# Performance work log

Measured on AMD Instinct MI355X. Metric: run time of the kernel, lower is better.

The kernel has to match this reference:

```python
import jax, jax.numpy as jnp
import numpy as np

N, E, G = 50000, 600000, 512   # nodes, edges, graphs
F, D, L = 128, 128, 3          # in_features, hidden dim, num_gc_layers
ED = D * L                      # embedding_dim (readout='concat')
C = 1.0                         # curvature
MIN_NORM = 1e-15
BALL_EPS = 4e-3                 # hgcn PoincareBall proj eps for float32


def _logmap0(p, c):
    sc = jnp.sqrt(c)
    n = jnp.clip(jnp.linalg.norm(p, axis=-1, keepdims=True), MIN_NORM, None)
    return p / (sc * n) * jnp.arctanh(jnp.clip(sc * n, -1 + 1e-15, 1 - 1e-15))


def _expmap0(u, c):
    sc = jnp.sqrt(c)
    n = jnp.clip(jnp.linalg.norm(u, axis=-1, keepdims=True), MIN_NORM, None)
    return jnp.tanh(sc * n) * u / (sc * n)


def _proj(x, c):
    n = jnp.clip(jnp.linalg.norm(x, axis=-1, keepdims=True), MIN_NORM, None)
    maxn = (1.0 - BALL_EPS) / jnp.sqrt(c)
    return jnp.where(n > maxn, x / n * maxn, x)


def _gcn(x, W, b, src, dst):
    h = x @ W
    deg = jax.ops.segment_sum(jnp.ones_like(dst, dtype=h.dtype), dst, num_segments=N) + 1.0
    dinv = deg ** -0.5
    msg = h[src] * (dinv[src] * dinv[dst])[:, None]           # [E, D]
    agg = jax.ops.segment_sum(msg, dst, num_segments=N) + h * (dinv * dinv)[:, None]
    return agg + b


def _encoder(x, Ws, bs, src, dst, batch):
    xs = []
    for W, b in zip(Ws, bs):
        x = jax.nn.relu(_gcn(x, W, b, src, dst))
        xs.append(x)
    # readout='concat' with global_add_pool
    g = jnp.concatenate([jax.ops.segment_sum(h, batch, num_segments=G) for h in xs], axis=1)
    return g, jnp.concatenate(xs, axis=1)


def _mlp(x, W1, W2):  # proj_head: Linear (no bias), ReLU, Linear (no bias)
    return jax.nn.relu(x @ W1) @ W2


def setup_inputs() -> dict:
    key = jax.random.key(0)
    ks = jax.random.split(key, 24)

    def xav(k, i, o):
        return jax.random.normal(k, (i, o), dtype=jnp.float32) * np.float32(np.sqrt(2.0 / (i + o)))

    inp = {
        'x':   jax.random.normal(ks[0], (N, F), dtype=jnp.float32) * 1e-3,  # points inside the ball
        'x_s': jax.random.normal(ks[1], (N, F), dtype=jnp.float32) * 1e-3,
        'src': jax.random.randint(ks[2], (E,), 0, N, dtype=jnp.int32),
        'dst': jax.random.randint(ks[3], (E,), 0, N, dtype=jnp.int32),
        'batch': jnp.sort(jax.random.randint(ks[4], (N,), 0, G, dtype=jnp.int32)),
        # feature-branch GCN encoder
        'Wf0': xav(ks[5], F, D), 'Wf1': xav(ks[6], D, D), 'Wf2': xav(ks[7], D, D),
        'bf0': jnp.zeros((D,), jnp.float32), 'bf1': jnp.zeros((D,), jnp.float32), 'bf2': jnp.zeros((D,), jnp.float32),
        # structure-branch GCN encoder
        'Ws0': xav(ks[8], F, D), 'Ws1': xav(ks[9], D, D), 'Ws2': xav(ks[10], D, D),
        'bs0': jnp.zeros((D,), jnp.float32), 'bs1': jnp.zeros((D,), jnp.float32), 'bs2': jnp.zeros((D,), jnp.float32),
        # proj heads (biases removed by init_emb)
        'P1': xav(ks[11], ED, ED), 'P2': xav(ks[12], ED, ED),
        'G1': xav(ks[13], 2 * ED, ED), 'G2': xav(ks[14], ED, ED),
    }
    return inp


def reference(x, x_s, Wf0, Wf1, Wf2, bf0, bf1, bf2, Ws0, Ws1, Ws2, bs0, bs1, bs2, P1, P2, G1, G2, src, dst, batch):
    xt_f = _logmap0(x, C)
    xt_s = _logmap0(x_s, C)
    g_f, n_f = _encoder(xt_f, (Wf0, Wf1, Wf2), (bf0, bf1, bf2), src, dst, batch)
    g_s, n_s = _encoder(xt_s, (Ws0, Ws1, Ws2), (bs0, bs1, bs2), src, dst, batch)
    g = _mlp(jnp.concatenate((g_f, g_s), axis=1), G1, G2)
    e = lambda t: _proj(_expmap0(t, C), C)
    return (e(g), e(_mlp(g_f, P1, P2)), e(_mlp(n_f, P1, P2)), e(_mlp(g_s, P1, P2)), e(_mlp(n_s, P1, P2)))
```

## Files before the change

### kernel.cpp

```cpp
#include <hip/hip_runtime.h>
#include <math.h>

#define N_NODES 50000
#define N_EDGES 600000
#define N_GRAPHS 512
#define F_IN 128
#define D_HID 128
#define EDIM 384
#define M_ALL (N_NODES + N_GRAPHS)

typedef __attribute__((ext_vector_type(8))) short bf16x8;
typedef __attribute__((ext_vector_type(4))) float f32x4;

static __device__ __forceinline__ float wave_reduce_sum(float s) {
#pragma unroll
  for (int off = 32; off > 0; off >>= 1) s += __shfl_xor(s, off, 64);
  return s;
}

static __device__ __forceinline__ short f2b(float f) {
  unsigned u = __float_as_uint(f);
  unsigned r = (u + 0x7FFFu + ((u >> 16) & 1u)) >> 16;
  return (short)r;
}

static __device__ __forceinline__ float b2f(short s) {
  return __uint_as_float(((unsigned)(unsigned short)s) << 16);
}


__global__ void hist_kernel(const int* __restrict__ dst, int* __restrict__ cnt) {
  int i = blockIdx.x * blockDim.x + threadIdx.x;
  if (i < N_EDGES) atomicAdd(&cnt[dst[i]], 1);
}

__global__ void gptr_kernel(const int* __restrict__ batch, int* __restrict__ gptr) {
  int g = blockIdx.x * blockDim.x + threadIdx.x;
  if (g > N_GRAPHS) return;
  int lo = 0, hi = N_NODES;
  while (lo < hi) { int mid = (lo + hi) >> 1; if (batch[mid] < g) lo = mid + 1; else hi = mid; }
  gptr[g] = lo;
}


#define SCAN_BS 256
#define SCAN_NB ((N_NODES + SCAN_BS - 1) / SCAN_BS)

__global__ __launch_bounds__(SCAN_BS) void scan1_kernel(const int* __restrict__ cnt,
                                                        int* __restrict__ row_ptr,
                                                        int* __restrict__ bsum) {
  __shared__ int wsum[4];
  int tid = threadIdx.x, lane = tid & 63, wid = tid >> 6;
  int idx = blockIdx.x * SCAN_BS + tid;
  int v = (idx < N_NODES) ? cnt[idx] : 0;
  int x = v;
#pragma unroll
  for (int off = 1; off < 64; off <<= 1) {
    int t = __shfl_up(x, off, 64);
    if (lane >= off) x += t;
  }
  if (lane == 63) wsum[wid] = x;
  __syncthreads();
  int pre = 0, tot = 0;
#pragma unroll
  for (int w = 0; w < 4; ++w) { int s = wsum[w]; tot += s; if (w < wid) pre += s; }
  if (idx < N_NODES) row_ptr[idx + 1] = x + pre;
  if (tid == 0) bsum[blockIdx.x] = tot;
}

__global__ __launch_bounds__(SCAN_BS) void scan2_kernel(const int* __restrict__ bsum,
                                                        int* __restrict__ boffs) {
  __shared__ int wsum[4];
  int tid = threadIdx.x, lane = tid & 63, wid = tid >> 6;
  int v = (tid < SCAN_NB) ? bsum[tid] : 0;
  int x = v;
#pragma unroll
  for (int off = 1; off < 64; off <<= 1) {
    int t = __shfl_up(x, off, 64);
    if (lane >= off) x += t;
  }
  if (lane == 63) wsum[wid] = x;
  __syncthreads();
  int pre = 0;
#pragma unroll
  for (int w = 0; w < 4; ++w) { int s = wsum[w]; if (w < wid) pre += s; }
  if (tid < SCAN_NB) boffs[tid] = x + pre - v;
}

__global__ __launch_bounds__(SCAN_BS) void scan3_kernel(const int* __restrict__ cnt,
                                                        const int* __restrict__ boffs,
                                                        int* __restrict__ row_ptr,
                                                        int* __restrict__ cursor) {
  int idx = blockIdx.x * SCAN_BS + threadIdx.x;
  if (idx >= N_NODES) return;
  int val = row_ptr[idx + 1] + boffs[blockIdx.x];
  row_ptr[idx + 1] = val;
  cursor[idx] = val - cnt[idx];
  if (idx == 0) row_ptr[0] = 0;
}

__global__ void dinv_kernel(const int* __restrict__ cnt, float* __restrict__ dinv) {
  int i = blockIdx.x * blockDim.x + threadIdx.x;
  if (i < N_NODES) dinv[i] = 1.0f / sqrtf((float)(cnt[i] + 1));
}

__global__ void scatter_kernel(const int* __restrict__ src, const int* __restrict__ dst,
                               const float* __restrict__ dinv, int* __restrict__ cursor,
                               int* __restrict__ col, float* __restrict__ ew) {
  int e = blockIdx.x * blockDim.x + threadIdx.x;
  if (e >= N_EDGES) return;
  int s = src[e], d = dst[e];
  int pos = atomicAdd(&cursor[d], 1);
  col[pos] = s;
  ew[pos] = dinv[s] * dinv[d];
}


struct WcSeg { const float* W; short* Wt; int K; int Nc; };
struct WcArgs { WcSeg seg[10]; };

__global__ void wconv_all_kernel(WcArgs a) {
  int sidx = blockIdx.y;
  WcSeg s = a.seg[sidx];
  int i = blockIdx.x * blockDim.x + threadIdx.x;
  if (i >= s.K * s.Nc) return;
  int k = i / s.Nc, n = i - k * s.Nc;
  s.Wt[(size_t)n * s.K + k] = f2b(s.W[i]);
}


__global__ __launch_bounds__(256) void logmap2_kernel(const float* __restrict__ x,
                                                      const float* __restrict__ x_s,
                                                      short* __restrict__ Ab) {
  int w = blockIdx.x * 4 + (threadIdx.x >> 6);
  int lane = threadIdx.x & 63;
  if (w >= 2 * N_NODES) return;
  int br = (w >= N_NODES) ? 1 : 0;
  int row = br ? (w - N_NODES) : w;
  const float* xr = (br ? x_s : x) + (size_t)row * F_IN;
  float2 v = *(const float2*)(xr + lane * 2);
  float s = wave_reduce_sum(v.x * v.x + v.y * v.y);
  float n = sqrtf(s);
  float nc = fmaxf(n, 1e-15f);
  float f = atanhf(fminf(nc, 0.9999999f)) / nc;
  short2 o; o.x = f2b(v.x * f); o.y = f2b(v.y * f);
  *(short2*)(Ab + (size_t)row * 256 + br * 128 + lane * 2) = o;
}


__global__ __launch_bounds__(256) void agg2_kernel(const short* __restrict__ Xin, int lda,
                                                   const float* __restrict__ dinv,
                                                   const int* __restrict__ row_ptr,
                                                   const int* __restrict__ col,
                                                   const float* __restrict__ ew,
                                                   short* __restrict__ Xa) {
  int node = blockIdx.x * 4 + (threadIdx.x >> 6);
  int lane = threadIdx.x & 63;
  if (node >= N_NODES) return;
  float di = dinv[node];
  float wsf = di * di;
  short4 sv = *(const short4*)(Xin + (size_t)node * lda + lane * 4);
  float a0 = b2f(sv.x) * wsf, a1 = b2f(sv.y) * wsf, a2 = b2f(sv.z) * wsf, a3 = b2f(sv.w) * wsf;
  int s = row_ptr[node], e = row_ptr[node + 1];
  int j = s;
  for (; j + 4 <= e; j += 4) {
    int c0 = col[j], c1 = col[j + 1], c2 = col[j + 2], c3 = col[j + 3];
    float w0 = ew[j], w1 = ew[j + 1], w2 = ew[j + 2], w3 = ew[j + 3];
    short4 v0 = *(const short4*)(Xin + (size_t)c0 * lda + lane * 4);
    short4 v1 = *(const short4*)(Xin + (size_t)c1 * lda + lane * 4);
    short4 v2 = *(const short4*)(Xin + (size_t)c2 * lda + lane * 4);
    short4 v3 = *(const short4*)(Xin + (size_t)c3 * lda + lane * 4);
    a0 += b2f(v0.x) * w0; a1 += b2f(v0.y) * w0; a2 += b2f(v0.z) * w0; a3 += b2f(v0.w) * w0;
    a0 += b2f(v1.x) * w1; a1 += b2f(v1.y) * w1; a2 += b2f(v1.z) * w1; a3 += b2f(v1.w) * w1;
    a0 += b2f(v2.x) * w2; a1 += b2f(v2.y) * w2; a2 += b2f(v2.z) * w2; a3 += b2f(v2.w) * w2;
    a0 += b2f(v3.x) * w3; a1 += b2f(v3.y) * w3; a2 += b2f(v3.z) * w3; a3 += b2f(v3.w) * w3;
  }
  for (; j < e; ++j) {
    float w0 = ew[j];
    short4 v0 = *(const short4*)(Xin + (size_t)col[j] * lda + lane * 4);
    a0 += b2f(v0.x) * w0; a1 += b2f(v0.y) * w0; a2 += b2f(v0.z) * w0; a3 += b2f(v0.w) * w0;
  }
  short4 o; o.x = f2b(a0); o.y = f2b(a1); o.z = f2b(a2); o.w = f2b(a3);
  *(short4*)(Xa + (size_t)node * 256 + lane * 4) = o;
}


#define LDK 40

struct GemmZArgs {
  const short* A[2];
  const short* Bt[2];
  const float* bias[2];
  short* Cb[2];
  float* Cf[2];
  float* Cf2[2];
  int lda, ldc, M, Nc, K, kexp, do_relu, split;
};

__global__ __launch_bounds__(256) void mfma_gemmz_kernel(GemmZArgs g) {
  __shared__ __align__(16) short As[128 * LDK];
  __shared__ __align__(16) short Bs[128 * LDK];
  int z = blockIdx.z;
  const short* __restrict__ A = g.A[z];
  const short* __restrict__ Bt = g.Bt[z];
  int tid = threadIdx.x;
  int wave = tid >> 6, lane = tid & 63;
  int wr = (wave >> 1) * 64, wc = (wave & 1) * 64;
  int q = lane >> 4, m = lane & 15;
  int row0 = blockIdx.x * 128, col0 = blockIdx.y * 128;
  f32x4 acc[4][4] = {};
  for (int k0 = 0; k0 < g.K; k0 += 32) {
#pragma unroll
    for (int p = 0; p < 2; ++p) {
      int idx = p * 256 + tid;
      int r = idx >> 2, kc = (idx & 3) * 8;
      int gr = row0 + r;
      int kk = k0 + kc;
      int acol = g.kexp ? (kk + ((kk >> 7) << 7)) : kk;
      float4 v = make_float4(0.f, 0.f, 0.f, 0.f);
      if (gr < g.M) v = *(const float4*)(A + (size_t)gr * g.lda + acol);
      *(float4*)(As + r * LDK + kc) = v;
      float4 w = *(const float4*)(Bt + (size_t)(col0 + r) * g.K + kk);
      *(float4*)(Bs + r * LDK + kc) = w;
    }
    __syncthreads();
    bf16x8 af[4], bfr[4];
#pragma unroll
    for (int i = 0; i < 4; ++i) {
      af[i]  = *(const bf16x8*)(As + (wr + i * 16 + m) * LDK + q * 8);
      bfr[i] = *(const bf16x8*)(Bs + (wc + i * 16 + m) * LDK + q * 8);
    }
#pragma unroll
    for (int i = 0; i < 4; ++i)
#pragma unroll
      for (int j = 0; j < 4; ++j)
        acc[i][j] = __builtin_amdgcn_mfma_f32_16x16x32_bf16(af[i], bfr[j], acc[i][j], 0, 0, 0);
    __syncthreads();
  }
  const float* __restrict__ bias = g.bias[z];
  short* __restrict__ Cb = g.Cb[z];
  float* __restrict__ Cf = g.Cf[z];
  float* __restrict__ Cf2 = g.Cf2[z];
#pragma unroll
  for (int i = 0; i < 4; ++i) {
#pragma unroll
    for (int r = 0; r < 4; ++r) {
      int rr = row0 + wr + i * 16 + q * 4 + r;
      if (rr >= g.M) continue;
#pragma unroll
      for (int j = 0; j < 4; ++j) {
        int cc = col0 + wc + j * 16 + m;
        float v = acc[i][j][r];
        if (bias) v += bias[cc];
        if (g.do_relu) v = fmaxf(v, 0.0f);
        if (Cb) Cb[(size_t)rr * g.ldc + cc] = f2b(v);
        else if (rr < g.split) Cf[(size_t)rr * g.Nc + cc] = v;
        else Cf2[(size_t)(rr - g.split) * g.Nc + cc] = v;
      }
    }
  }
}


__global__ __launch_bounds__(768) void pool2_kernel(const short* __restrict__ NB,
                                                    const int* __restrict__ gptr,
                                                    short* __restrict__ GCb,
                                                    short* __restrict__ nbappend) {
  int g = blockIdx.x, t = threadIdx.x;
  int s = gptr[g], e = gptr[g + 1];
  float acc = 0.0f;
  for (int i = s; i < e; ++i) acc += b2f(NB[(size_t)i * 768 + t]);
  short bv = f2b(acc);
  int l = t >> 8, rem = t & 255, b = rem >> 7, c = rem & 127;
  GCb[(size_t)g * 768 + b * 384 + l * 128 + c] = bv;
  nbappend[(size_t)g * 768 + t] = bv;
}


__global__ __launch_bounds__(256) void exp_proj_kernel(float* __restrict__ y, int nrows) {
  int row = blockIdx.x * 4 + (threadIdx.x >> 6);
  int lane = threadIdx.x & 63;
  if (row >= nrows) return;
  float* p = y + (size_t)row * EDIM;
  float v[6];
  float s = 0.0f;
#pragma unroll
  for (int j = 0; j < 6; ++j) { v[j] = p[lane + j * 64]; s += v[j] * v[j]; }
  s = wave_reduce_sum(s);
  float n = fmaxf(sqrtf(s), 1e-15f);
  float th = tanhf(n);
  float f = th / n;
  float n2 = fmaxf(th, 1e-15f);
  const float maxn = 1.0f - 4e-3f;
  if (n2 > maxn) f *= maxn / n2;
#pragma unroll
  for (int j = 0; j < 6; ++j) p[lane + j * 64] = v[j] * f;
}


extern "C" void kernel_launch(void* const* d_in, const int* in_sizes, int n_in,
                              void* d_out, int out_size, void* d_ws, size_t ws_size,
                              hipStream_t stream) {
  (void)in_sizes; (void)n_in; (void)out_size; (void)ws_size;
  const float* x   = (const float*)d_in[0];
  const float* x_s = (const float*)d_in[1];
  const int* src   = (const int*)d_in[2];
  const int* dst   = (const int*)d_in[3];
  const int* batch = (const int*)d_in[4];
  const float* Wf[3] = {(const float*)d_in[5], (const float*)d_in[6], (const float*)d_in[7]};
  const float* bf[3] = {(const float*)d_in[8], (const float*)d_in[9], (const float*)d_in[10]};
  const float* Wsb[3] = {(const float*)d_in[11], (const float*)d_in[12], (const float*)d_in[13]};
  const float* bs[3] = {(const float*)d_in[14], (const float*)d_in[15], (const float*)d_in[16]};
  const float* P1 = (const float*)d_in[17];
  const float* P2 = (const float*)d_in[18];
  const float* G1 = (const float*)d_in[19];
  const float* G2 = (const float*)d_in[20];
  float* out = (float*)d_out;

  char* w = (char*)d_ws;
  auto alloc = [&](size_t bytes) {
    char* p = w;
    w += (bytes + 255) & ~(size_t)255;
    return p;
  };
  short* HIDb = (short*)alloc((size_t)M_ALL * 384 * 2);
  short* Ab   = HIDb;
  short* Xa   = (short*)alloc((size_t)N_NODES * 256 * 2);
  short* NB   = (short*)alloc((size_t)M_ALL * 768 * 2);
  int* cnt    = (int*)alloc((size_t)N_NODES * 4);
  int* row_ptr= (int*)alloc((size_t)(N_NODES + 1) * 4);
  int* cursor = (int*)alloc((size_t)N_NODES * 4);
  float* dinv = (float*)alloc((size_t)N_NODES * 4);
  int* col    = (int*)alloc((size_t)N_EDGES * 4);
  float* ew   = (float*)alloc((size_t)N_EDGES * 4);
  int* gptr   = (int*)alloc((size_t)(N_GRAPHS + 1) * 4);
  int* bsum   = (int*)alloc(256 * 4);
  int* boffs  = (int*)alloc(256 * 4);
  short* GCb  = (short*)alloc((size_t)N_GRAPHS * 768 * 2);
  short* GHb  = (short*)alloc((size_t)N_GRAPHS * 384 * 2);
  short* P1t  = (short*)alloc((size_t)EDIM * EDIM * 2);
  short* P2t  = (short*)alloc((size_t)EDIM * EDIM * 2);
  short* G1t  = (short*)alloc((size_t)768 * EDIM * 2);
  short* G2t  = (short*)alloc((size_t)EDIM * EDIM * 2);
  short* Wft[3], *Wst[3];
  for (int l = 0; l < 3; ++l) {
    Wft[l] = (short*)alloc((size_t)128 * 128 * 2);
    Wst[l] = (short*)alloc((size_t)128 * 128 * 2);
  }

  hipMemsetAsync(cnt, 0, (size_t)N_NODES * 4, stream);
  hist_kernel<<<(N_EDGES + 255) / 256, 256, 0, stream>>>(dst, cnt);
  gptr_kernel<<<(N_GRAPHS + 256) / 256, 256, 0, stream>>>(batch, gptr);
  scan1_kernel<<<SCAN_NB, SCAN_BS, 0, stream>>>(cnt, row_ptr, bsum);
  scan2_kernel<<<1, SCAN_BS, 0, stream>>>(bsum, boffs);
  scan3_kernel<<<SCAN_NB, SCAN_BS, 0, stream>>>(cnt, boffs, row_ptr, cursor);
  dinv_kernel<<<(N_NODES + 255) / 256, 256, 0, stream>>>(cnt, dinv);
  scatter_kernel<<<(N_EDGES + 255) / 256, 256, 0, stream>>>(src, dst, dinv, cursor, col, ew);

  {
    WcArgs wa;
    wa.seg[0] = {P1, P1t, EDIM, EDIM};
    wa.seg[1] = {P2, P2t, EDIM, EDIM};
    wa.seg[2] = {G1, G1t, 768, EDIM};
    wa.seg[3] = {G2, G2t, EDIM, EDIM};
    for (int l = 0; l < 3; ++l) {
      wa.seg[4 + l] = {Wf[l], Wft[l], 128, 128};
      wa.seg[7 + l] = {Wsb[l], Wst[l], 128, 128};
    }
    wconv_all_kernel<<<dim3((768 * EDIM + 255) / 256, 10), 256, 0, stream>>>(wa);
  }

  const size_t OUT0 = 0;
  const size_t OUT1 = (size_t)N_GRAPHS * EDIM;
  const size_t OUT2 = OUT1 + (size_t)N_GRAPHS * EDIM;
  const size_t OUT3 = OUT2 + (size_t)N_NODES * EDIM;

  const int gx_layer = (N_NODES + 127) / 128;
  const int gx_mfma  = (M_ALL + 127) / 128;
  const int gx_agg   = (N_NODES + 3) / 4;

  logmap2_kernel<<<(2 * N_NODES + 3) / 4, 256, 0, stream>>>(x, x_s, Ab);

  const short* cur = Ab;
  int clda = 256;
  for (int l = 0; l < 3; ++l) {
    agg2_kernel<<<gx_agg, 256, 0, stream>>>(cur, clda, dinv, row_ptr, col, ew, Xa);
    GemmZArgs ga = {};
    ga.A[0] = Xa;        ga.A[1] = Xa + 128;
    ga.Bt[0] = Wft[l];   ga.Bt[1] = Wst[l];
    ga.bias[0] = bf[l];  ga.bias[1] = bs[l];
    ga.Cb[0] = NB + l * 256;        ga.Cb[1] = NB + l * 256 + 128;
    ga.lda = 256; ga.ldc = 768; ga.M = N_NODES; ga.Nc = 128; ga.K = 128;
    ga.kexp = 0; ga.do_relu = 1; ga.split = 0;
    mfma_gemmz_kernel<<<dim3(gx_layer, 1, 2), 256, 0, stream>>>(ga);
    cur = NB + l * 256;
    clda = 768;
  }

  pool2_kernel<<<N_GRAPHS, 768, 0, stream>>>(NB, gptr, GCb, NB + (size_t)N_NODES * 768);

  float* ghead_out[2] = {out + OUT1, out + OUT3};
  float* node_out[2]  = {out + OUT2, out + OUT3 + (size_t)N_GRAPHS * EDIM};
  for (int b = 0; b < 2; ++b) {
    GemmZArgs h1 = {};
    h1.A[0] = h1.A[1] = NB + b * 128;
    h1.Bt[0] = h1.Bt[1] = P1t;
    h1.Cb[0] = h1.Cb[1] = HIDb;
    h1.lda = 768; h1.ldc = 384; h1.M = M_ALL; h1.Nc = EDIM; h1.K = EDIM;
    h1.kexp = 1; h1.do_relu = 1; h1.split = 0;
    mfma_gemmz_kernel<<<dim3(gx_mfma, 3, 1), 256, 0, stream>>>(h1);

    GemmZArgs h2 = {};
    h2.A[0] = h2.A[1] = HIDb;
    h2.Bt[0] = h2.Bt[1] = P2t;
    h2.Cf[0] = h2.Cf[1] = node_out[b];
    h2.Cf2[0] = h2.Cf2[1] = ghead_out[b];
    h2.lda = 384; h2.ldc = 0; h2.M = M_ALL; h2.Nc = EDIM; h2.K = EDIM;
    h2.kexp = 0; h2.do_relu = 0; h2.split = N_NODES;
    mfma_gemmz_kernel<<<dim3(gx_mfma, 3, 1), 256, 0, stream>>>(h2);
  }

  exp_proj_kernel<<<(2 * M_ALL + 3) / 4, 256, 0, stream>>>(out + OUT1, 2 * M_ALL);

  const int gx_g = (N_GRAPHS + 127) / 128;
  {
    GemmZArgs g1 = {};
    g1.A[0] = g1.A[1] = GCb;
    g1.Bt[0] = g1.Bt[1] = G1t;
    g1.Cb[0] = g1.Cb[1] = GHb;
    g1.lda = 768; g1.ldc = 384; g1.M = N_GRAPHS; g1.Nc = EDIM; g1.K = 768;
    g1.kexp = 0; g1.do_relu = 1; g1.split = 0;
    mfma_gemmz_kernel<<<dim3(gx_g, 3, 1), 256, 0, stream>>>(g1);

    GemmZArgs g2 = {};
    g2.A[0] = g2.A[1] = GHb;
    g2.Bt[0] = g2.Bt[1] = G2t;
    g2.Cf[0] = g2.Cf[1] = out + OUT0;
    g2.Cf2[0] = g2.Cf2[1] = out + OUT0;
    g2.lda = 384; g2.ldc = 0; g2.M = N_GRAPHS; g2.Nc = EDIM; g2.K = EDIM;
    g2.kexp = 0; g2.do_relu = 0; g2.split = 1 << 30;
    mfma_gemmz_kernel<<<dim3(gx_g, 3, 1), 256, 0, stream>>>(g2);
  }
  exp_proj_kernel<<<(N_GRAPHS + 3) / 4, 256, 0, stream>>>(out + OUT0, N_GRAPHS);
}
```

Baseline: 870.0 us.

## Merge preprocessing kernels and batch both projection-head branches into single launches

Folds the memset and gptr search into one init kernel. It also merges scan2 into scan3, with each block reducing the preceding block sums itself, and moves the dinv computation into scan3. The two per-branch projection-head GEMM pairs become single launches using the z grid dimension, with a doubled hidden buffer. The two exp_proj launches become one launch covering all output rows. The aim is to cut kernel launch count and serialization and to give the head GEMMs a larger grid, at the cost of more workspace memory.

New measurement: 844.8 us. 1.03x faster.

```diff
diff --git a/kernel.cpp b/kernel.cpp
--- a/kernel.cpp
+++ b/kernel.cpp
@@ -18,6 +18,12 @@
   return s;
 }
 
+static __device__ __forceinline__ int wave_reduce_sum_i(int s) {
+#pragma unroll
+  for (int off = 32; off > 0; off >>= 1) s += __shfl_xor(s, off, 64);
+  return s;
+}
+
 static __device__ __forceinline__ short f2b(float f) {
   unsigned u = __float_as_uint(f);
   unsigned r = (u + 0x7FFFu + ((u >> 16) & 1u)) >> 16;
@@ -29,22 +35,25 @@
 }
 
 
+#define SCAN_BS 256
+#define SCAN_NB ((N_NODES + SCAN_BS - 1) / SCAN_BS)
+
+__global__ __launch_bounds__(SCAN_BS) void init_kernel(const int* __restrict__ batch,
+                                                       int* __restrict__ cnt,
+                                                       int* __restrict__ gptr) {
+  int i = blockIdx.x * SCAN_BS + threadIdx.x;
+  if (i < N_NODES) cnt[i] = 0;
+  if (i <= N_GRAPHS) {
+    int lo = 0, hi = N_NODES;
+    while (lo < hi) { int mid = (lo + hi) >> 1; if (batch[mid] < i) lo = mid + 1; else hi = mid; }
+    gptr[i] = lo;
+  }
+}
+
 __global__ void hist_kernel(const int* __restrict__ dst, int* __restrict__ cnt) {
   int i = blockIdx.x * blockDim.x + threadIdx.x;
   if (i < N_EDGES) atomicAdd(&cnt[dst[i]], 1);
 }
-
-__global__ void gptr_kernel(const int* __restrict__ batch, int* __restrict__ gptr) {
-  int g = blockIdx.x * blockDim.x + threadIdx.x;
-  if (g > N_GRAPHS) return;
-  int lo = 0, hi = N_NODES;
-  while (lo < hi) { int mid = (lo + hi) >> 1; if (batch[mid] < g) lo = mid + 1; else hi = mid; }
-  gptr[g] = lo;
-}
-
-
-#define SCAN_BS 256
-#define SCAN_NB ((N_NODES + SCAN_BS - 1) / SCAN_BS)
 
 __global__ __launch_bounds__(SCAN_BS) void scan1_kernel(const int* __restrict__ cnt,
                                                         int* __restrict__ row_ptr,
@@ -68,40 +77,27 @@
   if (tid == 0) bsum[blockIdx.x] = tot;
 }
 
-__global__ __launch_bounds__(SCAN_BS) void scan2_kernel(const int* __restrict__ bsum,
-                                                        int* __restrict__ boffs) {
-  __shared__ int wsum[4];
+__global__ __launch_bounds__(SCAN_BS) void scan3_kernel(const int* __restrict__ cnt,
+                                                        const int* __restrict__ bsum,
+                                                        int* __restrict__ row_ptr,
+                                                        int* __restrict__ cursor,
+                                                        float* __restrict__ dinv) {
+  __shared__ int ws[4];
   int tid = threadIdx.x, lane = tid & 63, wid = tid >> 6;
-  int v = (tid < SCAN_NB) ? bsum[tid] : 0;
-  int x = v;
-#pragma unroll
-  for (int off = 1; off < 64; off <<= 1) {
-    int t = __shfl_up(x, off, 64);
-    if (lane >= off) x += t;
-  }
-  if (lane == 63) wsum[wid] = x;
+  int v = 0;
+  if (tid < SCAN_NB && tid < blockIdx.x) v = bsum[tid];
+  v = wave_reduce_sum_i(v);
+  if (lane == 0) ws[wid] = v;
   __syncthreads();
-  int pre = 0;
-#pragma unroll
-  for (int w = 0; w < 4; ++w) { int s = wsum[w]; if (w < wid) pre += s; }
-  if (tid < SCAN_NB) boffs[tid] = x + pre - v;
-}
-
-__global__ __launch_bounds__(SCAN_BS) void scan3_kernel(const int* __restrict__ cnt,
-                                                        const int* __restrict__ boffs,
-                                                        int* __restrict__ row_ptr,
-                                                        int* __restrict__ cursor) {
-  int idx = blockIdx.x * SCAN_BS + threadIdx.x;
+  int boff = ws[0] + ws[1] + ws[2] + ws[3];
+  int idx = blockIdx.x * SCAN_BS + tid;
   if (idx >= N_NODES) return;
-  int val = row_ptr[idx + 1] + boffs[blockIdx.x];
+  int val = row_ptr[idx + 1] + boff;
   row_ptr[idx + 1] = val;
-  cursor[idx] = val - cnt[idx];
+  int c = cnt[idx];
+  cursor[idx] = val - c;
+  dinv[idx] = 1.0f / sqrtf((float)(c + 1));
   if (idx == 0) row_ptr[0] = 0;
-}
-
-__global__ void dinv_kernel(const int* __restrict__ cnt, float* __restrict__ dinv) {
-  int i = blockIdx.x * blockDim.x + threadIdx.x;
-  if (i < N_NODES) dinv[i] = 1.0f / sqrtf((float)(cnt[i] + 1));
 }
 
 __global__ void scatter_kernel(const int* __restrict__ src, const int* __restrict__ dst,
@@ -323,39 +319,29 @@
     w += (bytes + 255) & ~(size_t)255;
     return p;
   };
-  short* HIDb = (short*)alloc((size_t)M_ALL * 384 * 2);
-  short* Ab   = HIDb;
-  short* Xa   = (short*)alloc((size_t)N_NODES * 256 * 2);
-  short* NB   = (short*)alloc((size_t)M_ALL * 768 * 2);
-  int* cnt    = (int*)alloc((size_t)N_NODES * 4);
-  int* row_ptr= (int*)alloc((size_t)(N_NODES + 1) * 4);
-  int* cursor = (int*)alloc((size_t)N_NODES * 4);
-  float* dinv = (float*)alloc((size_t)N_NODES * 4);
-  int* col    = (int*)alloc((size_t)N_EDGES * 4);
-  float* ew   = (float*)alloc((size_t)N_EDGES * 4);
-  int* gptr   = (int*)alloc((size_t)(N_GRAPHS + 1) * 4);
-  int* bsum   = (int*)alloc(256 * 4);
-  int* boffs  = (int*)alloc(256 * 4);
-  short* GCb  = (short*)alloc((size_t)N_GRAPHS * 768 * 2);
-  short* GHb  = (short*)alloc((size_t)N_GRAPHS * 384 * 2);
-  short* P1t  = (short*)alloc((size_t)EDIM * EDIM * 2);
-  short* P2t  = (short*)alloc((size_t)EDIM * EDIM * 2);
-  short* G1t  = (short*)alloc((size_t)768 * EDIM * 2);
-  short* G2t  = (short*)alloc((size_t)EDIM * EDIM * 2);
+  short* HIDb2 = (short*)alloc((size_t)2 * M_ALL * 384 * 2);
+  short* Ab    = HIDb2;
+  short* Xa    = (short*)alloc((size_t)N_NODES * 256 * 2);
+  short* NB    = (short*)alloc((size_t)M_ALL * 768 * 2);
+  int* cnt     = (int*)alloc((size_t)N_NODES * 4);
+  int* row_ptr = (int*)alloc((size_t)(N_NODES + 1) * 4);
+  int* cursor  = (int*)alloc((size_t)N_NODES * 4);
+  float* dinv  = (float*)alloc((size_t)N_NODES * 4);
+  int* col     = (int*)alloc((size_t)N_EDGES * 4);
+  float* ew    = (float*)alloc((size_t)N_EDGES * 4);
+  int* gptr    = (int*)alloc((size_t)(N_GRAPHS + 1) * 4);
+  int* bsum    = (int*)alloc(256 * 4);
+  short* GCb   = (short*)alloc((size_t)N_GRAPHS * 768 * 2);
+  short* GHb   = (short*)alloc((size_t)N_GRAPHS * 384 * 2);
+  short* P1t   = (short*)alloc((size_t)EDIM * EDIM * 2);
+  short* P2t   = (short*)alloc((size_t)EDIM * EDIM * 2);
+  short* G1t   = (short*)alloc((size_t)768 * EDIM * 2);
+  short* G2t   = (short*)alloc((size_t)EDIM * EDIM * 2);
   short* Wft[3], *Wst[3];
   for (int l = 0; l < 3; ++l) {
     Wft[l] = (short*)alloc((size_t)128 * 128 * 2);
     Wst[l] = (short*)alloc((size_t)128 * 128 * 2);
   }
-
-  hipMemsetAsync(cnt, 0, (size_t)N_NODES * 4, stream);
-  hist_kernel<<<(N_EDGES + 255) / 256, 256, 0, stream>>>(dst, cnt);
-  gptr_kernel<<<(N_GRAPHS + 256) / 256, 256, 0, stream>>>(batch, gptr);
-  scan1_kernel<<<SCAN_NB, SCAN_BS, 0, stream>>>(cnt, row_ptr, bsum);
-  scan2_kernel<<<1, SCAN_BS, 0, stream>>>(bsum, boffs);
-  scan3_kernel<<<SCAN_NB, SCAN_BS, 0, stream>>>(cnt, boffs, row_ptr, cursor);
-  dinv_kernel<<<(N_NODES + 255) / 256, 256, 0, stream>>>(cnt, dinv);
-  scatter_kernel<<<(N_EDGES + 255) / 256, 256, 0, stream>>>(src, dst, dinv, cursor, col, ew);
 
   {
     WcArgs wa;
@@ -369,6 +355,12 @@
     }
     wconv_all_kernel<<<dim3((768 * EDIM + 255) / 256, 10), 256, 0, stream>>>(wa);
   }
+
+  init_kernel<<<SCAN_NB, SCAN_BS, 0, stream>>>(batch, cnt, gptr);
+  hist_kernel<<<(N_EDGES + 255) / 256, 256, 0, stream>>>(dst, cnt);
+  scan1_kernel<<<SCAN_NB, SCAN_BS, 0, stream>>>(cnt, row_ptr, bsum);
+  scan3_kernel<<<SCAN_NB, SCAN_BS, 0, stream>>>(cnt, bsum, row_ptr, cursor, dinv);
+  scatter_kernel<<<(N_EDGES + 255) / 256, 256, 0, stream>>>(src, dst, dinv, cursor, col, ew);
 
   const size_t OUT0 = 0;
   const size_t OUT1 = (size_t)N_GRAPHS * EDIM;
@@ -399,29 +391,6 @@
 
   pool2_kernel<<<N_GRAPHS, 768, 0, stream>>>(NB, gptr, GCb, NB + (size_t)N_NODES * 768);
 
-  float* ghead_out[2] = {out + OUT1, out + OUT3};
-  float* node_out[2]  = {out + OUT2, out + OUT3 + (size_t)N_GRAPHS * EDIM};
-  for (int b = 0; b < 2; ++b) {
-    GemmZArgs h1 = {};
-    h1.A[0] = h1.A[1] = NB + b * 128;
-    h1.Bt[0] = h1.Bt[1] = P1t;
-    h1.Cb[0] = h1.Cb[1] = HIDb;
-    h1.lda = 768; h1.ldc = 384; h1.M = M_ALL; h1.Nc = EDIM; h1.K = EDIM;
-    h1.kexp = 1; h1.do_relu = 1; h1.split = 0;
-    mfma_gemmz_kernel<<<dim3(gx_mfma, 3, 1), 256, 0, stream>>>(h1);
-
-    GemmZArgs h2 = {};
-    h2.A[0] = h2.A[1] = HIDb;
-    h2.Bt[0] = h2.Bt[1] = P2t;
-    h2.Cf[0] = h2.Cf[1] = node_out[b];
-    h2.Cf2[0] = h2.Cf2[1] = ghead_out[b];
-    h2.lda = 384; h2.ldc = 0; h2.M = M_ALL; h2.Nc = EDIM; h2.K = EDIM;
-    h2.kexp = 0; h2.do_relu = 0; h2.split = N_NODES;
-    mfma_gemmz_kernel<<<dim3(gx_mfma, 3, 1), 256, 0, stream>>>(h2);
-  }
-
-  exp_proj_kernel<<<(2 * M_ALL + 3) / 4, 256, 0, stream>>>(out + OUT1, 2 * M_ALL);
-
   const int gx_g = (N_GRAPHS + 127) / 128;
   {
     GemmZArgs g1 = {};
@@ -441,5 +410,28 @@
     g2.kexp = 0; g2.do_relu = 0; g2.split = 1 << 30;
     mfma_gemmz_kernel<<<dim3(gx_g, 3, 1), 256, 0, stream>>>(g2);
   }
-  exp_proj_kernel<<<(N_GRAPHS + 3) / 4, 256, 0, stream>>>(out + OUT0, N_GRAPHS);
-}
+
+  float* ghead_out[2] = {out + OUT1, out + OUT3};
+  float* node_out[2]  = {out + OUT2, out + OUT3 + (size_t)N_GRAPHS * EDIM};
+  {
+    GemmZArgs h1 = {};
+    h1.A[0] = NB;                 h1.A[1] = NB + 128;
+    h1.Bt[0] = h1.Bt[1] = P1t;
+    h1.Cb[0] = HIDb2;             h1.Cb[1] = HIDb2 + (size_t)M_ALL * 384;
+    h1.lda = 768; h1.ldc = 384; h1.M = M_ALL; h1.Nc = EDIM; h1.K = EDIM;
+    h1.kexp = 1; h1.do_relu = 1; h1.split = 0;
+    mfma_gemmz_kernel<<<dim3(gx_mfma, 3, 2), 256, 0, stream>>>(h1);
+
+    GemmZArgs h2 = {};
+    h2.A[0] = HIDb2;              h2.A[1] = HIDb2 + (size_t)M_ALL * 384;
+    h2.Bt[0] = h2.Bt[1] = P2t;
+    h2.Cf[0] = node_out[0];       h2.Cf[1] = node_out[1];
+    h2.Cf2[0] = ghead_out[0];     h2.Cf2[1] = ghead_out[1];
+    h2.lda = 384; h2.ldc = 0; h2.M = M_ALL; h2.Nc = EDIM; h2.K = EDIM;
+    h2.kexp = 0; h2.do_relu = 0; h2.split = N_NODES;
+    mfma_gemmz_kernel<<<dim3(gx_mfma, 3, 2), 256, 0, stream>>>(h2);
+  }
+
+  const int nrows_exp = N_GRAPHS + 2 * M_ALL;
+  exp_proj_kernel<<<(nrows_exp + 3) / 4, 256, 0, stream>>>(out + OUT0, nrows_exp);
+}
```
